# Performance work log

Measured on AMD Instinct MI355X. Metric: run time of the kernel, lower is better.

## Reference

```python
import jax, jax.numpy as jnp
import numpy as np

B, H, W, C = 32, 32, 32, 256


def setup_inputs() -> dict:
    key = jax.random.key(0)
    k1, k2 = jax.random.split(key)
    feats1 = jax.random.normal(k1, (B, H, W, C), dtype=jnp.float32)
    feats2 = jax.random.normal(k2, (B, H, W, C), dtype=jnp.float32)
    return {"feats1": feats1, "feats2": feats2}


def reference(feats1, feats2):
    # Training path of LocalFeatureLoss (trainflag=True)
    b, h, w, c = feats1.shape
    l = h * w
    q = feats1.reshape(b, l, c)  # queries: (B, l, C)
    p = feats2.reshape(b, l, c)  # preds:   (B, l, C)
    # M[b, a, j] = <p[b,a], q[b,j]>  == fm2 @ fm1.T per batch
    M = jnp.einsum('bac,bjc->baj', p, q)  # (B, l_pred, l_query)
    max1 = jnp.argmax(M, axis=1)  # (B, l_q): best pred index for each query token
    max2 = jnp.argmax(M, axis=2)  # (B, l_p): best query index for each pred token
    # mutual nearest-neighbor check: m[b, j] = max2[b, max1[b, j]]
    m = jnp.take_along_axis(max2, max1, axis=1)  # (B, l_q)
    valid = jnp.arange(l)[None, :] == m          # (B, l_q) bool
    # gather matched pred descriptors and compute per-pair similarity
    matched_p = jnp.take_along_axis(p, max1[..., None], axis=1)  # (B, l_q, C)
    sims = jnp.sum(q * matched_p, axis=-1)                        # (B, l_q)
    cnt = jnp.sum(valid, axis=1).astype(sims.dtype)               # (B,)
    # mean over mutual NN pairs (torch mean over idx1)
    similarity = jnp.sum(jnp.where(valid, sims, 0.0), axis=1) / jnp.maximum(cnt, 1.0)
    return similarity
```

## Files before the change

### kernel.cpp

```cpp
#include <hip/hip_runtime.h>
#include <hip/hip_bf16.h>

#define BATCH 32
#define L 1024
#define CD 256
#define BM 128
#define BN 128
#define BK 64
#define NRT (L / BM)
#define NCT (L / BN)

typedef __bf16 bf16x8 __attribute__((ext_vector_type(8)));
typedef __bf16 bf16x4 __attribute__((ext_vector_type(4)));
typedef float  f32x4  __attribute__((ext_vector_type(4)));

__device__ __forceinline__ unsigned int enc_f32(float f) {
    unsigned int u = __float_as_uint(f);
    return ((int)u < 0) ? ~u : (u | 0x80000000u);
}
__device__ __forceinline__ float dec_f32(unsigned int u) {
    u = (u & 0x80000000u) ? (u & 0x7FFFFFFFu) : ~u;
    return __uint_as_float(u);
}
__device__ __forceinline__ unsigned long long pmax(unsigned long long a, unsigned long long b) {
    return a > b ? a : b;
}
__device__ __forceinline__ bf16x4 cvt4(float4 v) {
    bf16x4 o;
    o[0] = (__bf16)v.x; o[1] = (__bf16)v.y; o[2] = (__bf16)v.z; o[3] = (__bf16)v.w;
    return o;
}

__global__ __launch_bounds__(512, 4) void mm_argmax_kernel(
    const float* __restrict__ qg,
    const float* __restrict__ pg,
    unsigned long long* __restrict__ colpart,
    unsigned long long* __restrict__ rowpart)
{
    __shared__ __bf16 sA[BM * BK];
    __shared__ __bf16 sB[BN * BK];
    __shared__ unsigned long long sRow[2][BM];
    __shared__ unsigned long long sCol[4][BN];

    const int tid = threadIdx.x;
    const int bid = blockIdx.x;
    const int b    = bid & 31;
    const int tile = bid >> 5;
    const int rt   = tile >> 3;
    const int ct   = tile & 7;
    const int row0 = rt * BM;
    const int col0 = ct * BN;

    const int lane = tid & 63;
    const int w    = tid >> 6;
    const int wm   = w >> 1;
    const int wn   = w & 1;
    const int quad = lane >> 4;
    const int l16  = lane & 15;

    const float* pA = pg + ((size_t)b * L + row0) * CD;
    const float* pB = qg + ((size_t)b * L + col0) * CD;

    const int sr = tid >> 4;
    const int sl = tid & 15;

    f32x4 acc[2][4];
    #pragma unroll
    for (int tm = 0; tm < 2; ++tm)
        #pragma unroll
        for (int tn = 0; tn < 4; ++tn) acc[tm][tn] = (f32x4){0.f, 0.f, 0.f, 0.f};

    float4 pfA[4], pfB[4];
    #pragma unroll
    for (int p = 0; p < 4; ++p) {
        pfA[p] = *(const float4*)(pA + (size_t)(p * 32 + sr) * CD + sl * 4);
        pfB[p] = *(const float4*)(pB + (size_t)(p * 32 + sr) * CD + sl * 4);
    }

    for (int step = 0; step < 4; ++step) {
        if (step) __syncthreads();
        #pragma unroll
        for (int p = 0; p < 4; ++p) {
            const int row = p * 32 + sr;
            const int idx = row * BK + (((sl >> 1) ^ (row & 7)) << 3) + ((sl & 1) << 2);
            *(bf16x4*)&sA[idx] = cvt4(pfA[p]);
            *(bf16x4*)&sB[idx] = cvt4(pfB[p]);
        }
        if (step < 3) {
            const int k0 = (step + 1) * BK;
            #pragma unroll
            for (int p = 0; p < 4; ++p) {
                pfA[p] = *(const float4*)(pA + (size_t)(p * 32 + sr) * CD + k0 + sl * 4);
                pfB[p] = *(const float4*)(pB + (size_t)(p * 32 + sr) * CD + k0 + sl * 4);
            }
        }
        __syncthreads();
        #pragma unroll
        for (int kk = 0; kk < 2; ++kk) {
            const int sw = ((kk * 4 + quad) ^ (l16 & 7)) << 3;
            bf16x8 a0 = *(const bf16x8*)&sA[(wm * 32      + l16) * BK + sw];
            bf16x8 a1 = *(const bf16x8*)&sA[(wm * 32 + 16 + l16) * BK + sw];
            bf16x8 b0 = *(const bf16x8*)&sB[(wn * 64      + l16) * BK + sw];
            bf16x8 b1 = *(const bf16x8*)&sB[(wn * 64 + 16 + l16) * BK + sw];
            bf16x8 b2 = *(const bf16x8*)&sB[(wn * 64 + 32 + l16) * BK + sw];
            bf16x8 b3 = *(const bf16x8*)&sB[(wn * 64 + 48 + l16) * BK + sw];
            acc[0][0] = __builtin_amdgcn_mfma_f32_16x16x32_bf16(a0, b0, acc[0][0], 0, 0, 0);
            acc[0][1] = __builtin_amdgcn_mfma_f32_16x16x32_bf16(a0, b1, acc[0][1], 0, 0, 0);
            acc[0][2] = __builtin_amdgcn_mfma_f32_16x16x32_bf16(a0, b2, acc[0][2], 0, 0, 0);
            acc[0][3] = __builtin_amdgcn_mfma_f32_16x16x32_bf16(a0, b3, acc[0][3], 0, 0, 0);
            acc[1][0] = __builtin_amdgcn_mfma_f32_16x16x32_bf16(a1, b0, acc[1][0], 0, 0, 0);
            acc[1][1] = __builtin_amdgcn_mfma_f32_16x16x32_bf16(a1, b1, acc[1][1], 0, 0, 0);
            acc[1][2] = __builtin_amdgcn_mfma_f32_16x16x32_bf16(a1, b2, acc[1][2], 0, 0, 0);
            acc[1][3] = __builtin_amdgcn_mfma_f32_16x16x32_bf16(a1, b3, acc[1][3], 0, 0, 0);
        }
    }

    const int a_base = row0 + wm * 32 + quad * 4;
    const int j_base = col0 + wn * 64 + l16;

    #pragma unroll
    for (int tn = 0; tn < 4; ++tn) {
        float cv = acc[0][tn][0];
        int   ca = a_base;
        #pragma unroll
        for (int tm = 0; tm < 2; ++tm)
            #pragma unroll
            for (int r = 0; r < 4; ++r) {
                if (tm == 0 && r == 0) continue;
                const float v = acc[tm][tn][r];
                const int   a = a_base + tm * 16 + r;
                if (v > cv) { cv = v; ca = a; }
            }
        unsigned long long pk =
            ((unsigned long long)enc_f32(cv) << 32) | (unsigned int)(~(unsigned int)ca);
        pk = pmax(pk, __shfl_xor(pk, 16));
        pk = pmax(pk, __shfl_xor(pk, 32));
        if (quad == 0) sCol[wm][wn * 64 + tn * 16 + l16] = pk;
    }

    #pragma unroll
    for (int tm = 0; tm < 2; ++tm)
        #pragma unroll
        for (int r = 0; r < 4; ++r) {
            float rv = acc[tm][0][r];
            int   rj = j_base;
            #pragma unroll
            for (int tn = 1; tn < 4; ++tn) {
                const float v = acc[tm][tn][r];
                if (v > rv) { rv = v; rj = j_base + tn * 16; }
            }
            unsigned long long pk =
                ((unsigned long long)enc_f32(rv) << 32) | (unsigned int)(~(unsigned int)rj);
            pk = pmax(pk, __shfl_xor(pk, 1));
            pk = pmax(pk, __shfl_xor(pk, 2));
            pk = pmax(pk, __shfl_xor(pk, 4));
            pk = pmax(pk, __shfl_xor(pk, 8));
            if (l16 == 0) sRow[wn][wm * 32 + tm * 16 + quad * 4 + r] = pk;
        }

    __syncthreads();
    if (tid < BN) {
        unsigned long long c = pmax(pmax(sCol[0][tid], sCol[1][tid]),
                                    pmax(sCol[2][tid], sCol[3][tid]));
        colpart[((size_t)b * NRT + rt) * L + col0 + tid] = c;
        unsigned long long rr = pmax(sRow[0][tid], sRow[1][tid]);
        rowpart[((size_t)b * NCT + ct) * L + row0 + tid] = rr;
    }
}

__global__ __launch_bounds__(256) void reduce_kernel(
    const unsigned long long* __restrict__ colpart,
    const unsigned long long* __restrict__ rowpart,
    unsigned long long* __restrict__ bestc,
    int* __restrict__ max2)
{
    const int b   = blockIdx.x & 31;
    const int ch  = blockIdx.x >> 5;
    const int idx = ch * 256 + threadIdx.x;

    unsigned long long cb = 0ull;
    #pragma unroll
    for (int rt = 0; rt < NRT; ++rt)
        cb = pmax(cb, colpart[((size_t)b * NRT + rt) * L + idx]);
    bestc[(size_t)b * L + idx] = cb;

    unsigned long long rb = 0ull;
    #pragma unroll
    for (int ct = 0; ct < NCT; ++ct)
        rb = pmax(rb, rowpart[((size_t)b * NCT + ct) * L + idx]);
    max2[(size_t)b * L + idx] = (int)(~(unsigned int)rb) & (L - 1);
}

__global__ __launch_bounds__(256) void finalize_kernel(
    const unsigned long long* __restrict__ bestc,
    const int* __restrict__ max2,
    float* __restrict__ out)
{
    __shared__ int sMax2[L];
    __shared__ float sSum[4];
    __shared__ int sCnt[4];
    const int b = blockIdx.x;
    const int tid = threadIdx.x;

    for (int i = tid; i < L; i += 256) sMax2[i] = max2[(size_t)b * L + i];
    __syncthreads();

    float sum = 0.f;
    int cnt = 0;
    #pragma unroll
    for (int i = 0; i < 4; ++i) {
        const int j = tid + i * 256;
        const unsigned long long best = bestc[(size_t)b * L + j];
        const int a = (int)(~(unsigned int)best) & (L - 1);
        const float val = dec_f32((unsigned int)(best >> 32));
        if (sMax2[a] == j) { sum += val; ++cnt; }
    }
    #pragma unroll
    for (int o = 32; o >= 1; o >>= 1) {
        sum += __shfl_down(sum, o);
        cnt += __shfl_down(cnt, o);
    }
    if ((tid & 63) == 0) { sSum[tid >> 6] = sum; sCnt[tid >> 6] = cnt; }
    __syncthreads();
    if (tid == 0) {
        float S = sSum[0] + sSum[1] + sSum[2] + sSum[3];
        int   C = sCnt[0] + sCnt[1] + sCnt[2] + sCnt[3];
        out[b] = S / fmaxf((float)C, 1.0f);
    }
}

extern "C" void kernel_launch(void* const* d_in, const int* in_sizes, int n_in,
                              void* d_out, int out_size, void* d_ws, size_t ws_size,
                              hipStream_t stream) {
    const float* q = (const float*)d_in[0];
    const float* p = (const float*)d_in[1];
    float* out = (float*)d_out;

    unsigned long long* colpart = (unsigned long long*)d_ws;
    unsigned long long* rowpart = colpart + (size_t)BATCH * NRT * L;
    unsigned long long* bestc   = rowpart + (size_t)BATCH * NCT * L;
    int* max2 = (int*)(bestc + (size_t)BATCH * L);

    mm_argmax_kernel<<<BATCH * NRT * NCT, 512, 0, stream>>>(q, p, colpart, rowpart);
    reduce_kernel<<<BATCH * 4, 256, 0, stream>>>(colpart, rowpart, bestc, max2);
    finalize_kernel<<<BATCH, 256, 0, stream>>>(bestc, max2, out);
}
```

Measured before the change: 137.0 us.

## Double-buffer LDS tiles in matmul-argmax and fuse reduce into finalize kernel

```diff
diff --git a/kernel.cpp b/kernel.cpp
--- a/kernel.cpp
+++ b/kernel.cpp
@@ -31,14 +31,20 @@
     return o;
 }
 
+__device__ __forceinline__ void block_sync_lgkm() {
+    asm volatile("s_waitcnt lgkmcnt(0)" ::: "memory");
+    __builtin_amdgcn_s_barrier();
+    asm volatile("" ::: "memory");
+}
+
 __global__ __launch_bounds__(512, 4) void mm_argmax_kernel(
     const float* __restrict__ qg,
     const float* __restrict__ pg,
     unsigned long long* __restrict__ colpart,
     unsigned long long* __restrict__ rowpart)
 {
-    __shared__ __bf16 sA[BM * BK];
-    __shared__ __bf16 sB[BN * BK];
+    __shared__ __bf16 sA[2][BM * BK];
+    __shared__ __bf16 sB[2][BN * BK];
     __shared__ unsigned long long sRow[2][BM];
     __shared__ unsigned long long sCol[4][BN];
 
@@ -71,49 +77,69 @@
         for (int tn = 0; tn < 4; ++tn) acc[tm][tn] = (f32x4){0.f, 0.f, 0.f, 0.f};
 
     float4 pfA[4], pfB[4];
-    #pragma unroll
-    for (int p = 0; p < 4; ++p) {
-        pfA[p] = *(const float4*)(pA + (size_t)(p * 32 + sr) * CD + sl * 4);
-        pfB[p] = *(const float4*)(pB + (size_t)(p * 32 + sr) * CD + sl * 4);
-    }
-
-    for (int step = 0; step < 4; ++step) {
-        if (step) __syncthreads();
-        #pragma unroll
-        for (int p = 0; p < 4; ++p) {
-            const int row = p * 32 + sr;
-            const int idx = row * BK + (((sl >> 1) ^ (row & 7)) << 3) + ((sl & 1) << 2);
-            *(bf16x4*)&sA[idx] = cvt4(pfA[p]);
-            *(bf16x4*)&sB[idx] = cvt4(pfB[p]);
+
+    #define LOADS(k0)                                                          \
+        _Pragma("unroll")                                                      \
+        for (int p = 0; p < 4; ++p) {                                          \
+            pfA[p] = *(const float4*)(pA + (size_t)(p * 32 + sr) * CD + (k0) + sl * 4); \
+            pfB[p] = *(const float4*)(pB + (size_t)(p * 32 + sr) * CD + (k0) + sl * 4); \
         }
-        if (step < 3) {
-            const int k0 = (step + 1) * BK;
-            #pragma unroll
-            for (int p = 0; p < 4; ++p) {
-                pfA[p] = *(const float4*)(pA + (size_t)(p * 32 + sr) * CD + k0 + sl * 4);
-                pfB[p] = *(const float4*)(pB + (size_t)(p * 32 + sr) * CD + k0 + sl * 4);
-            }
+
+    #define STAGE(buf)                                                         \
+        _Pragma("unroll")                                                      \
+        for (int p = 0; p < 4; ++p) {                                          \
+            const int row_ = p * 32 + sr;                                      \
+            const int idx_ = row_ * BK + (((sl >> 1) ^ (row_ & 7)) << 3) + ((sl & 1) << 2); \
+            *(bf16x4*)&sA[buf][idx_] = cvt4(pfA[p]);                           \
+            *(bf16x4*)&sB[buf][idx_] = cvt4(pfB[p]);                           \
         }
-        __syncthreads();
-        #pragma unroll
-        for (int kk = 0; kk < 2; ++kk) {
-            const int sw = ((kk * 4 + quad) ^ (l16 & 7)) << 3;
-            bf16x8 a0 = *(const bf16x8*)&sA[(wm * 32      + l16) * BK + sw];
-            bf16x8 a1 = *(const bf16x8*)&sA[(wm * 32 + 16 + l16) * BK + sw];
-            bf16x8 b0 = *(const bf16x8*)&sB[(wn * 64      + l16) * BK + sw];
-            bf16x8 b1 = *(const bf16x8*)&sB[(wn * 64 + 16 + l16) * BK + sw];
-            bf16x8 b2 = *(const bf16x8*)&sB[(wn * 64 + 32 + l16) * BK + sw];
-            bf16x8 b3 = *(const bf16x8*)&sB[(wn * 64 + 48 + l16) * BK + sw];
-            acc[0][0] = __builtin_amdgcn_mfma_f32_16x16x32_bf16(a0, b0, acc[0][0], 0, 0, 0);
-            acc[0][1] = __builtin_amdgcn_mfma_f32_16x16x32_bf16(a0, b1, acc[0][1], 0, 0, 0);
-            acc[0][2] = __builtin_amdgcn_mfma_f32_16x16x32_bf16(a0, b2, acc[0][2], 0, 0, 0);
-            acc[0][3] = __builtin_amdgcn_mfma_f32_16x16x32_bf16(a0, b3, acc[0][3], 0, 0, 0);
-            acc[1][0] = __builtin_amdgcn_mfma_f32_16x16x32_bf16(a1, b0, acc[1][0], 0, 0, 0);
-            acc[1][1] = __builtin_amdgcn_mfma_f32_16x16x32_bf16(a1, b1, acc[1][1], 0, 0, 0);
-            acc[1][2] = __builtin_amdgcn_mfma_f32_16x16x32_bf16(a1, b2, acc[1][2], 0, 0, 0);
-            acc[1][3] = __builtin_amdgcn_mfma_f32_16x16x32_bf16(a1, b3, acc[1][3], 0, 0, 0);
-        }
-    }
+
+    #define COMPUTE(buf)                                                       \
+        __builtin_amdgcn_s_setprio(1);                                         \
+        _Pragma("unroll")                                                      \
+        for (int kk = 0; kk < 2; ++kk) {                                       \
+            const int sw = ((kk * 4 + quad) ^ (l16 & 7)) << 3;                 \
+            bf16x8 a0 = *(const bf16x8*)&sA[buf][(wm * 32      + l16) * BK + sw]; \
+            bf16x8 a1 = *(const bf16x8*)&sA[buf][(wm * 32 + 16 + l16) * BK + sw]; \
+            bf16x8 b0 = *(const bf16x8*)&sB[buf][(wn * 64      + l16) * BK + sw]; \
+            bf16x8 b1 = *(const bf16x8*)&sB[buf][(wn * 64 + 16 + l16) * BK + sw]; \
+            bf16x8 b2 = *(const bf16x8*)&sB[buf][(wn * 64 + 32 + l16) * BK + sw]; \
+            bf16x8 b3 = *(const bf16x8*)&sB[buf][(wn * 64 + 48 + l16) * BK + sw]; \
+            acc[0][0] = __builtin_amdgcn_mfma_f32_16x16x32_bf16(a0, b0, acc[0][0], 0, 0, 0); \
+            acc[0][1] = __builtin_amdgcn_mfma_f32_16x16x32_bf16(a0, b1, acc[0][1], 0, 0, 0); \
+            acc[0][2] = __builtin_amdgcn_mfma_f32_16x16x32_bf16(a0, b2, acc[0][2], 0, 0, 0); \
+            acc[0][3] = __builtin_amdgcn_mfma_f32_16x16x32_bf16(a0, b3, acc[0][3], 0, 0, 0); \
+            acc[1][0] = __builtin_amdgcn_mfma_f32_16x16x32_bf16(a1, b0, acc[1][0], 0, 0, 0); \
+            acc[1][1] = __builtin_amdgcn_mfma_f32_16x16x32_bf16(a1, b1, acc[1][1], 0, 0, 0); \
+            acc[1][2] = __builtin_amdgcn_mfma_f32_16x16x32_bf16(a1, b2, acc[1][2], 0, 0, 0); \
+            acc[1][3] = __builtin_amdgcn_mfma_f32_16x16x32_bf16(a1, b3, acc[1][3], 0, 0, 0); \
+        }                                                                      \
+        __builtin_amdgcn_s_setprio(0);
+
+    LOADS(0);
+    STAGE(0);
+    LOADS(BK);
+    block_sync_lgkm();
+
+    COMPUTE(0);
+    STAGE(1);
+    LOADS(2 * BK);
+    block_sync_lgkm();
+
+    COMPUTE(1);
+    STAGE(0);
+    LOADS(3 * BK);
+    block_sync_lgkm();
+
+    COMPUTE(0);
+    STAGE(1);
+    block_sync_lgkm();
+
+    COMPUTE(1);
+
+    #undef LOADS
+    #undef STAGE
+    #undef COMPUTE
 
     const int a_base = row0 + wm * 32 + quad * 4;
     const int j_base = col0 + wn * 64 + l16;
@@ -168,63 +194,47 @@
     }
 }
 
-__global__ __launch_bounds__(256) void reduce_kernel(
+__global__ __launch_bounds__(1024) void finalize_kernel(
     const unsigned long long* __restrict__ colpart,
     const unsigned long long* __restrict__ rowpart,
-    unsigned long long* __restrict__ bestc,
-    int* __restrict__ max2)
-{
-    const int b   = blockIdx.x & 31;
-    const int ch  = blockIdx.x >> 5;
-    const int idx = ch * 256 + threadIdx.x;
-
-    unsigned long long cb = 0ull;
-    #pragma unroll
-    for (int rt = 0; rt < NRT; ++rt)
-        cb = pmax(cb, colpart[((size_t)b * NRT + rt) * L + idx]);
-    bestc[(size_t)b * L + idx] = cb;
-
-    unsigned long long rb = 0ull;
-    #pragma unroll
-    for (int ct = 0; ct < NCT; ++ct)
-        rb = pmax(rb, rowpart[((size_t)b * NCT + ct) * L + idx]);
-    max2[(size_t)b * L + idx] = (int)(~(unsigned int)rb) & (L - 1);
-}
-
-__global__ __launch_bounds__(256) void finalize_kernel(
-    const unsigned long long* __restrict__ bestc,
-    const int* __restrict__ max2,
     float* __restrict__ out)
 {
     __shared__ int sMax2[L];
-    __shared__ float sSum[4];
-    __shared__ int sCnt[4];
+    __shared__ float sSum[16];
+    __shared__ int sCnt[16];
     const int b = blockIdx.x;
-    const int tid = threadIdx.x;
-
-    for (int i = tid; i < L; i += 256) sMax2[i] = max2[(size_t)b * L + i];
+    const int j = threadIdx.x;
+
+    unsigned long long rb = 0ull;
+    #pragma unroll
+    for (int ct = 0; ct < NCT; ++ct)
+        rb = pmax(rb, rowpart[((size_t)b * NCT + ct) * L + j]);
+    sMax2[j] = (int)(~(unsigned int)rb) & (L - 1);
+
+    unsigned long long cb = 0ull;
+    #pragma unroll
+    for (int rt = 0; rt < NRT; ++rt)
+        cb = pmax(cb, colpart[((size_t)b * NRT + rt) * L + j]);
     __syncthreads();
 
-    float sum = 0.f;
-    int cnt = 0;
-    #pragma unroll
-    for (int i = 0; i < 4; ++i) {
-        const int j = tid + i * 256;
-        const unsigned long long best = bestc[(size_t)b * L + j];
-        const int a = (int)(~(unsigned int)best) & (L - 1);
-        const float val = dec_f32((unsigned int)(best >> 32));
-        if (sMax2[a] == j) { sum += val; ++cnt; }
-    }
+    const int a = (int)(~(unsigned int)cb) & (L - 1);
+    const float val = dec_f32((unsigned int)(cb >> 32));
+    const bool mut = (sMax2[a] == j);
+    float sum = mut ? val : 0.f;
+    int   cnt = mut ? 1 : 0;
+
     #pragma unroll
     for (int o = 32; o >= 1; o >>= 1) {
         sum += __shfl_down(sum, o);
         cnt += __shfl_down(cnt, o);
     }
-    if ((tid & 63) == 0) { sSum[tid >> 6] = sum; sCnt[tid >> 6] = cnt; }
+    if ((j & 63) == 0) { sSum[j >> 6] = sum; sCnt[j >> 6] = cnt; }
     __syncthreads();
-    if (tid == 0) {
-        float S = sSum[0] + sSum[1] + sSum[2] + sSum[3];
-        int   C = sCnt[0] + sCnt[1] + sCnt[2] + sCnt[3];
+    if (j == 0) {
+        float S = 0.f;
+        int   C = 0;
+        #pragma unroll
+        for (int i = 0; i < 16; ++i) { S += sSum[i]; C += sCnt[i]; }
         out[b] = S / fmaxf((float)C, 1.0f);
     }
 }
@@ -238,10 +248,7 @@
 
     unsigned long long* colpart = (unsigned long long*)d_ws;
     unsigned long long* rowpart = colpart + (size_t)BATCH * NRT * L;
-    unsigned long long* bestc   = rowpart + (size_t)BATCH * NCT * L;
-    int* max2 = (int*)(bestc + (size_t)BATCH * L);
 
     mm_argmax_kernel<<<BATCH * NRT * NCT, 512, 0, stream>>>(q, p, colpart, rowpart);
-    reduce_kernel<<<BATCH * 4, 256, 0, stream>>>(colpart, rowpart, bestc, max2);
-    finalize_kernel<<<BATCH, 256, 0, stream>>>(bestc, max2, out);
-}
+    finalize_kernel<<<BATCH, 1024, 0, stream>>>(colpart, rowpart, out);
+}
```

Result: faster. 129.4 us (-5.6%).
